# Performance work log

Measured on AMD Instinct MI355X. Metric: run time of the kernel, lower is better.

The kernel has to match this reference:

```python
import jax, jax.numpy as jnp
import numpy as np

B = 524288
H = 20          # heads
NUM_EX = 13     # embedding rows
EMB = 3         # embedding dim
FEAT_IN, FEAT_OUT = 3, 5
HEAD_IN, HEAD_HID = 8, 10


def setup_inputs() -> dict:
    key = jax.random.key(0)
    ks = jax.random.split(key, 12)
    e = jax.random.randint(ks[0], (B, H), 0, NUM_EX)
    f = jax.random.normal(ks[1], (B, H * FEAT_IN), dtype=jnp.float32)
    # embedding table; row 0 zeroed as in the torch __init__
    emb = jax.random.normal(ks[2], (NUM_EX, EMB), dtype=jnp.float32) * 0.1
    emb = emb.at[0].set(0.0)
    # features Linear(3 -> 5), stored as (in, out) so y = x @ Wf + bf
    Wf = jax.random.normal(ks[3], (FEAT_IN, FEAT_OUT), dtype=jnp.float32) * 0.5
    bf = jax.random.normal(ks[4], (FEAT_OUT,), dtype=jnp.float32) * 0.1
    # 20 parallel head MLPs, batched over the head axis
    W1 = jax.random.normal(ks[5], (H, HEAD_IN, HEAD_HID), dtype=jnp.float32) * 0.3
    b1 = jax.random.normal(ks[6], (H, HEAD_HID), dtype=jnp.float32) * 0.1
    W2 = jax.random.normal(ks[7], (H, HEAD_HID), dtype=jnp.float32) * 0.3
    b2 = jax.random.normal(ks[8], (H,), dtype=jnp.float32) * 0.1
    # output Linear(20 -> 1)
    Wo = jax.random.normal(ks[9], (H, 1), dtype=jnp.float32) * 0.3
    bo = jax.random.normal(ks[10], (1,), dtype=jnp.float32) * 0.1
    return {"e": e, "f": f, "emb": emb, "Wf": Wf, "bf": bf,
            "W1": W1, "b1": b1, "W2": W2, "b2": b2, "Wo": Wo, "bo": bo}


def reference(e, f, emb, Wf, bf, W1, b1, W2, b2, Wo, bo):
    ev = emb[e]                                    # (B, 20, 3) embedding lookup
    fv = f.reshape(-1, H, FEAT_IN) @ Wf + bf       # (B, 20, 5)
    x = jnp.concatenate([ev, fv], axis=2)          # (B, 20, 8)
    # all 20 heads as one batched matmul instead of a Python loop
    h1 = jax.nn.leaky_relu(jnp.einsum('bhi,hio->bho', x, W1) + b1)  # (B, 20, 10)
    h = jax.nn.softplus(jnp.einsum('bho,ho->bh', h1, W2) + b2)      # (B, 20)
    return h @ Wo + bo                             # (B, 1)
```

## Files before the change

### kernel.cpp

```cpp
#include <hip/hip_runtime.h>


#define HH   20
#define NEX  13
#define TST  12
#define WS_M 0
#define WS_T 640

__device__ __forceinline__ float softplus_fast(float x) {
    return fmaxf(x, 0.0f) + __logf(1.0f + __expf(-fabsf(x)));
}

__global__ void airfit_setup(const float* __restrict__ emb,
                             const float* __restrict__ Wf,
                             const float* __restrict__ bf,
                             const float* __restrict__ W1,
                             const float* __restrict__ b1,
                             float* __restrict__ ws)
{
    int t = blockIdx.x * 256 + threadIdx.x;
    if (t < HH * 3 * 10) {
        int h = t / 30, c = (t / 10) % 3, o = t % 10;
        float a = 0.0f;
        for (int q = 0; q < 5; ++q)
            a += Wf[c * 5 + q] * W1[(h * 8 + 3 + q) * 10 + o];
        ws[WS_M + (h * 3 + c) * 10 + o] = a;
    }
    if (t < HH * NEX * 10) {
        int h = t / (NEX * 10), idx = (t / 10) % NEX, o = t % 10;
        float a = b1[h * 10 + o];
        for (int i = 0; i < 3; ++i)
            a += emb[idx * 3 + i] * W1[(h * 8 + i) * 10 + o];
        for (int q = 0; q < 5; ++q)
            a += bf[q] * W1[(h * 8 + 3 + q) * 10 + o];
        ws[WS_T + (h * NEX + idx) * TST + o] = a;
    }
}

__global__ __launch_bounds__(256, 8) void airfit_kernel(
    const int*   __restrict__ e,   const float* __restrict__ f,
    const float* __restrict__ ws,  const float* __restrict__ W2,
    const float* __restrict__ b2,  const float* __restrict__ Wo,
    const float* __restrict__ bo,  float* __restrict__ out, int B)
{
    __shared__ float s_T[HH * NEX * TST];

    for (int t = threadIdx.x; t < HH * NEX * TST; t += 256)
        s_T[t] = ws[WS_T + t];
    __syncthreads();

    int item = blockIdx.x * 256 + threadIdx.x;
    if (item >= B) return;

    const int4*   ep = reinterpret_cast<const int4*>(e + (size_t)item * HH);
    const float4* fp = reinterpret_cast<const float4*>(f + (size_t)item * (HH * 3));
    const float* M = ws + WS_M;

    float acc = bo[0];

#pragma unroll
    for (int g = 0; g < 5; ++g) {
        int4   iv = ep[g];
        float4 fa = fp[3 * g + 0];
        float4 fb = fp[3 * g + 1];
        float4 fc = fp[3 * g + 2];
        int   ii[4]  = { iv.x, iv.y, iv.z, iv.w };
        float ff[12] = { fa.x, fa.y, fa.z, fa.w,
                         fb.x, fb.y, fb.z, fb.w,
                         fc.x, fc.y, fc.z, fc.w };

#pragma unroll
        for (int t = 0; t < 4; ++t) {
            const int h = 4 * g + t;
            const float* Trow = s_T + (h * NEX + ii[t]) * TST;
            float4 t0 = *reinterpret_cast<const float4*>(Trow);
            float4 t1 = *reinterpret_cast<const float4*>(Trow + 4);
            float2 t2 = *reinterpret_cast<const float2*>(Trow + 8);
            float pre[10] = { t0.x, t0.y, t0.z, t0.w,
                              t1.x, t1.y, t1.z, t1.w, t2.x, t2.y };

            float g0 = ff[3 * t + 0], g1 = ff[3 * t + 1], g2 = ff[3 * t + 2];
            float hacc = b2[h];
#pragma unroll
            for (int o = 0; o < 10; ++o) {
                float a = pre[o];
                a = fmaf(g0, M[(h * 3 + 0) * 10 + o], a);
                a = fmaf(g1, M[(h * 3 + 1) * 10 + o], a);
                a = fmaf(g2, M[(h * 3 + 2) * 10 + o], a);
                a = fmaxf(a, 0.01f * a);
                hacc = fmaf(a, W2[h * 10 + o], hacc);
            }
            acc = fmaf(softplus_fast(hacc), Wo[h], acc);
        }
    }

    out[item] = acc;
}

extern "C" void kernel_launch(void* const* d_in, const int* in_sizes, int n_in,
                              void* d_out, int out_size, void* d_ws, size_t ws_size,
                              hipStream_t stream) {
    const int*   e   = (const int*)  d_in[0];
    const float* f   = (const float*)d_in[1];
    const float* emb = (const float*)d_in[2];
    const float* Wf  = (const float*)d_in[3];
    const float* bf  = (const float*)d_in[4];
    const float* W1  = (const float*)d_in[5];
    const float* b1  = (const float*)d_in[6];
    const float* W2  = (const float*)d_in[7];
    const float* b2  = (const float*)d_in[8];
    const float* Wo  = (const float*)d_in[9];
    const float* bo  = (const float*)d_in[10];
    float* out = (float*)d_out;
    float* ws  = (float*)d_ws;

    int B = in_sizes[0] / HH;

    airfit_setup<<<11, 256, 0, stream>>>(emb, Wf, bf, W1, b1, ws);

    int blocks = (B + 255) / 256;
    airfit_kernel<<<blocks, 256, 0, stream>>>(e, f, ws, W2, b2, Wo, bo, out, B);
}
```

Baseline: 286.0 us.

## Stage per-block inputs through LDS with coalesced loads, pack indices to bytes

Each block now loads its contiguous slice of f and e cooperatively, with adjacent threads reading adjacent float4/int4 words, and stores them into shared memory transposed so each thread later reads its own item. The four embedding indices per group are packed into one 32-bit word. This replaces strided per-thread global loads, where each thread read a 240-byte row, with coalesced streaming. In exchange it uses about 60KB+ of LDS per block, adds a sync, and lowers the launch-bounds occupancy hint from 8 to 2, which reduces the latency hiding available.

```diff
diff --git a/kernel.cpp b/kernel.cpp
--- a/kernel.cpp
+++ b/kernel.cpp
@@ -37,42 +37,74 @@
     }
 }
 
-__global__ __launch_bounds__(256, 8) void airfit_kernel(
+__global__ __launch_bounds__(256, 2) void airfit_kernel(
     const int*   __restrict__ e,   const float* __restrict__ f,
     const float* __restrict__ ws,  const float* __restrict__ W2,
     const float* __restrict__ b2,  const float* __restrict__ Wo,
     const float* __restrict__ bo,  float* __restrict__ out, int B)
 {
-    __shared__ float s_T[HH * NEX * TST];
+    __shared__ float4       s_f4[15][257];
+    __shared__ unsigned int s_ep[256 * 5];
+    __shared__ float        s_T[HH * NEX * TST];
 
-    for (int t = threadIdx.x; t < HH * NEX * TST; t += 256)
+    const int tid  = threadIdx.x;
+    const int base = blockIdx.x * 256;
+    const int nIt  = min(256, B - base);
+
+    for (int t = tid; t < HH * NEX * TST; t += 256)
         s_T[t] = ws[WS_T + t];
+
+    {
+        const float4* fg = reinterpret_cast<const float4*>(f) + (size_t)base * 15;
+        const int total4 = nIt * 15;
+#pragma unroll
+        for (int k = 0; k < 15; ++k) {
+            int idx = tid + 256 * k;
+            if (idx < total4) {
+                float4 v = fg[idx];
+                int item = idx / 15, c4 = idx - item * 15;
+                s_f4[c4][item] = v;
+            }
+        }
+    }
+
+    {
+        const int4* eg = reinterpret_cast<const int4*>(e) + (size_t)base * 5;
+        const int total4 = nIt * 5;
+#pragma unroll
+        for (int k = 0; k < 5; ++k) {
+            int idx = tid + 256 * k;
+            if (idx < total4) {
+                int4 iv = eg[idx];
+                s_ep[idx] = (unsigned)iv.x | ((unsigned)iv.y << 8) |
+                            ((unsigned)iv.z << 16) | ((unsigned)iv.w << 24);
+            }
+        }
+    }
+
     __syncthreads();
 
-    int item = blockIdx.x * 256 + threadIdx.x;
-    if (item >= B) return;
-
-    const int4*   ep = reinterpret_cast<const int4*>(e + (size_t)item * HH);
-    const float4* fp = reinterpret_cast<const float4*>(f + (size_t)item * (HH * 3));
+    if (tid >= nIt) return;
     const float* M = ws + WS_M;
 
     float acc = bo[0];
 
 #pragma unroll
     for (int g = 0; g < 5; ++g) {
-        int4   iv = ep[g];
-        float4 fa = fp[3 * g + 0];
-        float4 fb = fp[3 * g + 1];
-        float4 fc = fp[3 * g + 2];
-        int   ii[4]  = { iv.x, iv.y, iv.z, iv.w };
-        float ff[12] = { fa.x, fa.y, fa.z, fa.w,
-                         fb.x, fb.y, fb.z, fb.w,
-                         fc.x, fc.y, fc.z, fc.w };
+        unsigned ep = s_ep[tid * 5 + g];
+        float4 fA = s_f4[3 * g + 0][tid];
+        float4 fB = s_f4[3 * g + 1][tid];
+        float4 fC = s_f4[3 * g + 2][tid];
+        float ff[12] = { fA.x, fA.y, fA.z, fA.w,
+                         fB.x, fB.y, fB.z, fB.w,
+                         fC.x, fC.y, fC.z, fC.w };
 
 #pragma unroll
         for (int t = 0; t < 4; ++t) {
             const int h = 4 * g + t;
-            const float* Trow = s_T + (h * NEX + ii[t]) * TST;
+            int idx = (ep >> (8 * t)) & 0xff;
+
+            const float* Trow = s_T + (h * NEX + idx) * TST;
             float4 t0 = *reinterpret_cast<const float4*>(Trow);
             float4 t1 = *reinterpret_cast<const float4*>(Trow + 4);
             float2 t2 = *reinterpret_cast<const float2*>(Trow + 8);
@@ -94,7 +126,7 @@
         }
     }
 
-    out[item] = acc;
+    out[base + tid] = acc;
 }
 
 extern "C" void kernel_launch(void* const* d_in, const int* in_sizes, int n_in,
```

After: 274.0 us. 4.2% less time.

## Use persistent blocks with double-buffered async LDS prefetch of features

Applied to the files above, without the earlier changes.

Replaces the one-block-per-256-items grid with 256 persistent blocks that loop over chunks. The feature rows for the next chunk are streamed into a second LDS buffer with global_load_lds while the current chunk is computed, and the two buffers alternate. The goal is to overlap feature loads with compute and to load the lookup table into LDS only once per block. The cost is a large LDS footprint that allows only one block, four waves, per CU, which cuts the latency hiding available for the index loads and other memory traffic.

```diff
diff --git a/kernel.cpp b/kernel.cpp
--- a/kernel.cpp
+++ b/kernel.cpp
@@ -6,6 +6,8 @@
 #define TST  12
 #define WS_M 0
 #define WS_T 640
+#define NB   256
+#define NT   256
 
 __device__ __forceinline__ float softplus_fast(float x) {
     return fmaxf(x, 0.0f) + __logf(1.0f + __expf(-fabsf(x)));
@@ -37,37 +39,48 @@
     }
 }
 
-__global__ __launch_bounds__(256, 8) void airfit_kernel(
-    const int*   __restrict__ e,   const float* __restrict__ f,
-    const float* __restrict__ ws,  const float* __restrict__ W2,
-    const float* __restrict__ b2,  const float* __restrict__ Wo,
-    const float* __restrict__ bo,  float* __restrict__ out, int B)
+__device__ __forceinline__ void prefetch_f(float4 (*__restrict__ sf)[4][64],
+                                           const float* __restrict__ f,
+                                           int chunk, int tid, int B)
 {
-    __shared__ float s_T[HH * NEX * TST];
+    const int w = tid >> 6, l = tid & 63;
+    int item = chunk * NT + (w << 6) + l;
+    if (item > B - 1) item = B - 1;
+    const float4* gp = reinterpret_cast<const float4*>(f) + (size_t)item * 15;
+#pragma unroll
+    for (int k = 0; k < 15; ++k) {
+        __builtin_amdgcn_global_load_lds(
+            (const __attribute__((address_space(1))) void*)(gp + k),
+            (__attribute__((address_space(3))) void*)(&sf[k][w][0]),
+            16, 0, 0);
+    }
+}
 
-    for (int t = threadIdx.x; t < HH * NEX * TST; t += 256)
-        s_T[t] = ws[WS_T + t];
-    __syncthreads();
-
-    int item = blockIdx.x * 256 + threadIdx.x;
+__device__ __forceinline__ void compute_chunk(
+    const float4 (*__restrict__ sf)[4][64],
+    const float* __restrict__ s_T, int chunk, int tid,
+    const int* __restrict__ e,  const float* __restrict__ M,
+    const float* __restrict__ W2, const float* __restrict__ b2,
+    const float* __restrict__ Wo, float bo0,
+    float* __restrict__ out, int B)
+{
+    const int w = tid >> 6, l = tid & 63;
+    const int item = chunk * NT + tid;
     if (item >= B) return;
 
-    const int4*   ep = reinterpret_cast<const int4*>(e + (size_t)item * HH);
-    const float4* fp = reinterpret_cast<const float4*>(f + (size_t)item * (HH * 3));
-    const float* M = ws + WS_M;
-
-    float acc = bo[0];
+    const int4* ep = reinterpret_cast<const int4*>(e + (size_t)item * HH);
+    float acc = bo0;
 
 #pragma unroll
     for (int g = 0; g < 5; ++g) {
-        int4   iv = ep[g];
-        float4 fa = fp[3 * g + 0];
-        float4 fb = fp[3 * g + 1];
-        float4 fc = fp[3 * g + 2];
-        int   ii[4]  = { iv.x, iv.y, iv.z, iv.w };
-        float ff[12] = { fa.x, fa.y, fa.z, fa.w,
-                         fb.x, fb.y, fb.z, fb.w,
-                         fc.x, fc.y, fc.z, fc.w };
+        int4 iv = ep[g];
+        int ii[4] = { iv.x, iv.y, iv.z, iv.w };
+        float4 fA = sf[3 * g + 0][w][l];
+        float4 fB = sf[3 * g + 1][w][l];
+        float4 fC = sf[3 * g + 2][w][l];
+        float ff[12] = { fA.x, fA.y, fA.z, fA.w,
+                         fB.x, fB.y, fB.z, fB.w,
+                         fC.x, fC.y, fC.z, fC.w };
 
 #pragma unroll
         for (int t = 0; t < 4; ++t) {
@@ -97,6 +110,42 @@
     out[item] = acc;
 }
 
+__global__ __launch_bounds__(NT) void airfit_kernel(
+    const int*   __restrict__ e,   const float* __restrict__ f,
+    const float* __restrict__ ws,  const float* __restrict__ W2,
+    const float* __restrict__ b2,  const float* __restrict__ Wo,
+    const float* __restrict__ bo,  float* __restrict__ out, int B)
+{
+    __shared__ float4 s_fA[15][4][64];
+    __shared__ float4 s_fB[15][4][64];
+    __shared__ float  s_T[HH * NEX * TST];
+
+    const int tid = threadIdx.x;
+    for (int t = tid; t < HH * NEX * TST; t += NT)
+        s_T[t] = ws[WS_T + t];
+
+    const int chunks = (B + NT - 1) / NT;
+    const float* M  = ws + WS_M;
+    const float bo0 = bo[0];
+
+    int c = blockIdx.x;
+    if (c < chunks) prefetch_f(s_fA, f, c, tid, B);
+    __syncthreads();
+
+    for (; c < chunks; c += 2 * NB) {
+        int cB = c + NB;
+        if (cB < chunks) prefetch_f(s_fB, f, cB, tid, B);
+        compute_chunk(s_fA, s_T, c, tid, e, M, W2, b2, Wo, bo0, out, B);
+        __syncthreads();
+
+        int cA = c + 2 * NB;
+        if (cA < chunks) prefetch_f(s_fA, f, cA, tid, B);
+        if (cB < chunks)
+            compute_chunk(s_fB, s_T, cB, tid, e, M, W2, b2, Wo, bo0, out, B);
+        __syncthreads();
+    }
+}
+
 extern "C" void kernel_launch(void* const* d_in, const int* in_sizes, int n_in,
                               void* d_out, int out_size, void* d_ws, size_t ws_size,
                               hipStream_t stream) {
@@ -117,7 +166,5 @@
     int B = in_sizes[0] / HH;
 
     airfit_setup<<<11, 256, 0, stream>>>(emb, Wf, bf, W1, b1, ws);
-
-    int blocks = (B + 255) / 256;
-    airfit_kernel<<<blocks, 256, 0, stream>>>(e, f, ws, W2, b2, Wo, bo, out, B);
+    airfit_kernel<<<NB, NT, 0, stream>>>(e, f, ws, W2, b2, Wo, bo, out, B);
 }
```

After: 285.6 us. No clear change (-0.1%).
